# Performance work log

Hardware: AMD Instinct MI355X
Metric: run time of the kernel (lower is better)

## Reference

```python
import jax, jax.numpy as jnp
import numpy as np

N_NODES = 100000
N_EDGES = 1600000
D_IN = 64
D_OUT = 64


def setup_inputs() -> dict:
    key = jax.random.key(0)
    k1, k2, k3, k4, k5 = jax.random.split(key, 5)
    features = jax.random.normal(k1, (N_NODES, D_IN), dtype=jnp.float32)
    edge_rows = jax.random.randint(k2, (N_EDGES,), 0, N_NODES, dtype=jnp.int32)
    edge_cols = jax.random.randint(k3, (N_EDGES,), 0, N_NODES, dtype=jnp.int32)
    edge_vals = jax.random.uniform(k4, (N_EDGES,), dtype=jnp.float32)
    # glorot_uniform init for the dense projection weight
    limit = np.sqrt(6.0 / (D_IN + D_OUT)).astype(np.float32)
    weight = jax.random.uniform(k5, (D_IN, D_OUT), dtype=jnp.float32,
                                minval=-limit, maxval=limit)
    return {"features": features, "edge_rows": edge_rows,
            "edge_cols": edge_cols, "edge_vals": edge_vals, "weight": weight}


def reference(features, edge_rows, edge_cols, edge_vals, weight):
    # SpMM: (adj @ features) via edge-list gather + segment_sum
    gathered = features[edge_cols] * edge_vals[:, None]        # [E, D_IN]
    agg = jax.ops.segment_sum(gathered, edge_rows,
                              num_segments=N_NODES)            # [N, D_IN]
    # Dense projection + ReLU
    return jax.nn.relu(agg @ weight)                           # [N, D_OUT]
```

## Files before the change

### kernel.cpp

```cpp
#include <hip/hip_runtime.h>

#define D 64
#define OVF_CAP 65536


__device__ inline unsigned short f32_to_bf16_rne(float x) {
    unsigned u = __float_as_uint(x);
    unsigned r = (u + 0x7FFFu + ((u >> 16) & 1u)) >> 16;
    return (unsigned short)r;
}

__global__ void f2bf_kernel(const float4* __restrict__ in,
                            ushort4* __restrict__ out, int n4) {
    int i = blockIdx.x * blockDim.x + threadIdx.x;
    int stride = gridDim.x * blockDim.x;
    for (; i < n4; i += stride) {
        float4 f = in[i];
        ushort4 u;
        u.x = f32_to_bf16_rne(f.x);
        u.y = f32_to_bf16_rne(f.y);
        u.z = f32_to_bf16_rne(f.z);
        u.w = f32_to_bf16_rne(f.w);
        out[i] = u;
    }
}

template <int SLOTS, int NSLICE>
__global__ void scatter_slot_kernel(const int* __restrict__ erows,
                                    const int* __restrict__ ecols,
                                    const float* __restrict__ evals,
                                    int* __restrict__ cnt,
                                    int2* __restrict__ pairs,
                                    int4* __restrict__ ovf,
                                    int* __restrict__ ovfCnt,
                                    int n_edges, int rows_per_slice) {
    const int slice = blockIdx.x & (NSLICE - 1);
    const int rlo   = slice * rows_per_slice;
    const int rhi   = rlo + rows_per_slice;
    const int sub   = blockIdx.x / NSLICE;
    const int t     = sub * blockDim.x + threadIdx.x;
    const int strid = (gridDim.x / NSLICE) * blockDim.x;

    auto handle = [&](int r, int c, float v) {
        if (r >= rlo && r < rhi) {
            int pos = atomicAdd(&cnt[r], 1);
            if (pos < SLOTS) {
                pairs[(size_t)r * SLOTS + pos] = make_int2(c, __float_as_int(v));
            } else {
                int oi = atomicAdd(ovfCnt, 1);
                if (oi < OVF_CAP) ovf[oi] = make_int4(r, c, __float_as_int(v), 0);
            }
        }
    };

    int e = t;
    for (; e + 3 * strid < n_edges; e += 4 * strid) {
        int e0 = e, e1 = e + strid, e2 = e + 2 * strid, e3 = e + 3 * strid;
        int   r0 = erows[e0], r1 = erows[e1], r2 = erows[e2], r3 = erows[e3];
        int   c0 = ecols[e0], c1 = ecols[e1], c2 = ecols[e2], c3 = ecols[e3];
        float v0 = evals[e0], v1 = evals[e1], v2 = evals[e2], v3 = evals[e3];
        handle(r0, c0, v0);
        handle(r1, c1, v1);
        handle(r2, c2, v2);
        handle(r3, c3, v3);
    }
    for (; e < n_edges; e += strid)
        handle(erows[e], ecols[e], evals[e]);
}

template <int SLOTS>
__global__ void __launch_bounds__(256)
fused_slot_bf16(const unsigned short* __restrict__ fb,
                const int* __restrict__ cnt, const int2* __restrict__ pairs,
                const float* __restrict__ W, const int* __restrict__ ovfCnt,
                float* __restrict__ out, int n_rows) {
    __shared__ float sW[D * D];
    __shared__ float srow[4][D];

    for (int i = threadIdx.x; i < D * D; i += 256)
        sW[i] = W[i];

    const int  w      = threadIdx.x >> 6;
    const int  lane   = threadIdx.x & 63;
    const int  row    = blockIdx.x * 4 + w;
    const bool doRelu = (*ovfCnt == 0);

    float acc = 0.0f;
    if (row < n_rows) {
        int m = min(cnt[row], SLOTS);
        int px = 0, py = 0;
        if (lane < m) {
            int2 p = pairs[(size_t)row * SLOTS + lane];
            px = p.x; py = p.y;
        }
        int k = 0;
        for (; k + 4 <= m; k += 4) {
            int c0 = __shfl(px, k + 0), b0 = __shfl(py, k + 0);
            int c1 = __shfl(px, k + 1), b1 = __shfl(py, k + 1);
            int c2 = __shfl(px, k + 2), b2 = __shfl(py, k + 2);
            int c3 = __shfl(px, k + 3), b3 = __shfl(py, k + 3);
            float f0 = __uint_as_float((unsigned)fb[(size_t)c0 * D + lane] << 16);
            float f1 = __uint_as_float((unsigned)fb[(size_t)c1 * D + lane] << 16);
            float f2 = __uint_as_float((unsigned)fb[(size_t)c2 * D + lane] << 16);
            float f3 = __uint_as_float((unsigned)fb[(size_t)c3 * D + lane] << 16);
            acc = fmaf(f0, __int_as_float(b0), acc);
            acc = fmaf(f1, __int_as_float(b1), acc);
            acc = fmaf(f2, __int_as_float(b2), acc);
            acc = fmaf(f3, __int_as_float(b3), acc);
        }
        for (; k < m; ++k) {
            int c = __shfl(px, k), b = __shfl(py, k);
            acc = fmaf(__uint_as_float((unsigned)fb[(size_t)c * D + lane] << 16),
                       __int_as_float(b), acc);
        }
    }
    srow[w][lane] = acc;
    __syncthreads();

    float o = 0.0f;
#pragma unroll
    for (int kk = 0; kk < D; ++kk)
        o = fmaf(srow[w][kk], sW[kk * D + lane], o);

    if (row < n_rows)
        out[(size_t)row * D + lane] = doRelu ? fmaxf(o, 0.0f) : o;
}

template <int SLOTS>
__global__ void __launch_bounds__(256)
fused_slot_f32(const float* __restrict__ feat, const int* __restrict__ cnt,
               const int2* __restrict__ pairs, const float* __restrict__ W,
               const int* __restrict__ ovfCnt, float* __restrict__ out,
               int n_rows) {
    __shared__ float sW[D * D];
    __shared__ float srow[4][D];
    for (int i = threadIdx.x; i < D * D; i += 256) sW[i] = W[i];
    const int  w      = threadIdx.x >> 6;
    const int  lane   = threadIdx.x & 63;
    const int  row    = blockIdx.x * 4 + w;
    const bool doRelu = (*ovfCnt == 0);
    float acc = 0.0f;
    if (row < n_rows) {
        int m = min(cnt[row], SLOTS);
        int px = 0, py = 0;
        if (lane < m) {
            int2 p = pairs[(size_t)row * SLOTS + lane];
            px = p.x; py = p.y;
        }
        int k = 0;
        for (; k + 4 <= m; k += 4) {
            int c0 = __shfl(px, k + 0), b0 = __shfl(py, k + 0);
            int c1 = __shfl(px, k + 1), b1 = __shfl(py, k + 1);
            int c2 = __shfl(px, k + 2), b2 = __shfl(py, k + 2);
            int c3 = __shfl(px, k + 3), b3 = __shfl(py, k + 3);
            float f0 = feat[(size_t)c0 * D + lane];
            float f1 = feat[(size_t)c1 * D + lane];
            float f2 = feat[(size_t)c2 * D + lane];
            float f3 = feat[(size_t)c3 * D + lane];
            acc = fmaf(f0, __int_as_float(b0), acc);
            acc = fmaf(f1, __int_as_float(b1), acc);
            acc = fmaf(f2, __int_as_float(b2), acc);
            acc = fmaf(f3, __int_as_float(b3), acc);
        }
        for (; k < m; ++k) {
            int c = __shfl(px, k), b = __shfl(py, k);
            acc = fmaf(feat[(size_t)c * D + lane], __int_as_float(b), acc);
        }
    }
    srow[w][lane] = acc;
    __syncthreads();
    float o = 0.0f;
#pragma unroll
    for (int kk = 0; kk < D; ++kk)
        o = fmaf(srow[w][kk], sW[kk * D + lane], o);
    if (row < n_rows)
        out[(size_t)row * D + lane] = doRelu ? fmaxf(o, 0.0f) : o;
}

__global__ void __launch_bounds__(256)
ovf_kernel(const float* __restrict__ feat, const float* __restrict__ W,
           const int4* __restrict__ ovf, const int* __restrict__ ovfCnt,
           float* __restrict__ out) {
    int n = *ovfCnt;
    if (n > OVF_CAP) n = OVF_CAP;
    if (n == 0) return;
    const int lane = threadIdx.x & 63;
    const int wave = (blockIdx.x * blockDim.x + threadIdx.x) >> 6;
    const int nw   = (gridDim.x * blockDim.x) >> 6;
    for (int i = wave; i < n; i += nw) {
        int4  e = ovf[i];
        float v = __int_as_float(e.z);
        float f = feat[(size_t)e.y * D + lane];
        float acc = 0.0f;
#pragma unroll
        for (int k = 0; k < D; ++k)
            acc = fmaf(__shfl(f, k), W[k * D + lane], acc);
        unsafeAtomicAdd(&out[(size_t)e.x * D + lane], v * acc);
    }
}

__global__ void relu_fix_kernel(float* __restrict__ out,
                                const int* __restrict__ ovfCnt, int n_elems) {
    if (*ovfCnt == 0) return;
    int i = blockIdx.x * blockDim.x + threadIdx.x;
    int stride = gridDim.x * blockDim.x;
    for (; i < n_elems; i += stride)
        out[i] = fmaxf(out[i], 0.0f);
}

__global__ void hist_kernel(const int* __restrict__ erows, int* __restrict__ cur,
                            int n_edges) {
    int i = blockIdx.x * blockDim.x + threadIdx.x;
    int stride = gridDim.x * blockDim.x;
    for (int e = i; e < n_edges; e += stride) atomicAdd(&cur[erows[e]], 1);
}

__global__ void __launch_bounds__(256)
scan_block_reduce(const int* __restrict__ cnt, int* __restrict__ bs, int n) {
    __shared__ int s[256];
    int i = blockIdx.x * 256 + threadIdx.x;
    s[threadIdx.x] = (i < n) ? cnt[i] : 0;
    __syncthreads();
    for (int off = 128; off > 0; off >>= 1) {
        if (threadIdx.x < (unsigned)off) s[threadIdx.x] += s[threadIdx.x + off];
        __syncthreads();
    }
    if (threadIdx.x == 0) bs[blockIdx.x] = s[0];
}

__global__ void __launch_bounds__(1024)
scan_top(int* __restrict__ bs, int nblk, int* __restrict__ rowStartN) {
    __shared__ int s[1024];
    int t = threadIdx.x;
    int x = (t < nblk) ? bs[t] : 0;
    s[t] = x;
    __syncthreads();
    for (int off = 1; off < 1024; off <<= 1) {
        int y = (t >= off) ? s[t - off] : 0;
        __syncthreads();
        s[t] += y;
        __syncthreads();
    }
    if (t < nblk) bs[t] = s[t] - x;
    if (t == 1023) *rowStartN = s[1023];
}

__global__ void __launch_bounds__(256)
scan_final(int* __restrict__ cur, const int* __restrict__ bs,
           int* __restrict__ rowStart, int n) {
    __shared__ int s[256];
    int t = threadIdx.x;
    int i = blockIdx.x * 256 + t;
    int x = (i < n) ? cur[i] : 0;
    s[t] = x;
    __syncthreads();
    for (int off = 1; off < 256; off <<= 1) {
        int y = (t >= off) ? s[t - off] : 0;
        __syncthreads();
        s[t] += y;
        __syncthreads();
    }
    int excl = s[t] - x + bs[blockIdx.x];
    if (i < n) { rowStart[i] = excl; cur[i] = excl; }
}

__global__ void scatter_kernel(const int* __restrict__ erows,
                               const int* __restrict__ ecols,
                               const float* __restrict__ evals,
                               int* __restrict__ cur, int2* __restrict__ pairs,
                               int n_edges) {
    int i = blockIdx.x * blockDim.x + threadIdx.x;
    int stride = gridDim.x * blockDim.x;
    for (int e = i; e < n_edges; e += stride) {
        int pos = atomicAdd(&cur[erows[e]], 1);
        pairs[pos] = make_int2(ecols[e], __float_as_int(evals[e]));
    }
}

__global__ void __launch_bounds__(256)
fused_kernel(const float* __restrict__ feat, const int* __restrict__ rowStart,
             const int2* __restrict__ pairs, const float* __restrict__ W,
             float* __restrict__ out, int n_rows) {
    __shared__ float sW[D * D];
    __shared__ float srow[4][D];
    for (int i = threadIdx.x; i < D * D; i += 256) sW[i] = W[i];
    const int w = threadIdx.x >> 6, lane = threadIdx.x & 63;
    const int row = blockIdx.x * 4 + w;
    float acc = 0.0f;
    if (row < n_rows) {
        int s = rowStart[row], e = rowStart[row + 1], i = s;
        for (; i + 4 <= e; i += 4) {
            int2 p0 = pairs[i + 0], p1 = pairs[i + 1];
            int2 p2 = pairs[i + 2], p3 = pairs[i + 3];
            float f0 = feat[(size_t)p0.x * D + lane];
            float f1 = feat[(size_t)p1.x * D + lane];
            float f2 = feat[(size_t)p2.x * D + lane];
            float f3 = feat[(size_t)p3.x * D + lane];
            acc = fmaf(f0, __int_as_float(p0.y), acc);
            acc = fmaf(f1, __int_as_float(p1.y), acc);
            acc = fmaf(f2, __int_as_float(p2.y), acc);
            acc = fmaf(f3, __int_as_float(p3.y), acc);
        }
        for (; i < e; ++i) {
            int2 p = pairs[i];
            acc = fmaf(feat[(size_t)p.x * D + lane], __int_as_float(p.y), acc);
        }
    }
    srow[w][lane] = acc;
    __syncthreads();
    float o = 0.0f;
#pragma unroll
    for (int k = 0; k < D; ++k) o = fmaf(srow[w][k], sW[k * D + lane], o);
    if (row < n_rows) out[(size_t)row * D + lane] = fmaxf(o, 0.0f);
}

__global__ void agg_kernel(const float* __restrict__ feat,
                           const int* __restrict__ erows,
                           const int* __restrict__ ecols,
                           const float* __restrict__ evals,
                           float* __restrict__ agg, int n_edges) {
    int gid = blockIdx.x * blockDim.x + threadIdx.x;
    int group = gid >> 4, lane4 = gid & 15;
    int stride = (gridDim.x * blockDim.x) >> 4;
    for (int e = group; e < n_edges; e += stride) {
        int r = erows[e], c = ecols[e];
        float v = evals[e];
        const float4 f = *reinterpret_cast<const float4*>(feat + (size_t)c * D + lane4 * 4);
        float* dst = agg + (size_t)r * D + lane4 * 4;
        unsafeAtomicAdd(dst + 0, f.x * v);
        unsafeAtomicAdd(dst + 1, f.y * v);
        unsafeAtomicAdd(dst + 2, f.z * v);
        unsafeAtomicAdd(dst + 3, f.w * v);
    }
}

__global__ void __launch_bounds__(256)
proj_kernel(const float* __restrict__ agg, const float* __restrict__ W,
            float* __restrict__ out, int n_rows) {
    __shared__ float sW[D * D];
    __shared__ float srow[4][D];
    for (int i = threadIdx.x; i < D * D; i += 256) sW[i] = W[i];
    __syncthreads();
    const int rg = threadIdx.x >> 6, j = threadIdx.x & 63;
    for (int row0 = blockIdx.x * 4; row0 < n_rows; row0 += gridDim.x * 4) {
        int r = row0 + rg;
        float v = (r < n_rows) ? agg[(size_t)r * D + j] : 0.0f;
        srow[rg][j] = v;
        __syncthreads();
        float acc = 0.0f;
#pragma unroll
        for (int k = 0; k < D; ++k) acc = fmaf(srow[rg][k], sW[k * D + j], acc);
        if (r < n_rows) out[(size_t)r * D + j] = fmaxf(acc, 0.0f);
        __syncthreads();
    }
}

extern "C" void kernel_launch(void* const* d_in, const int* in_sizes, int n_in,
                              void* d_out, int out_size, void* d_ws, size_t ws_size,
                              hipStream_t stream) {
    const float* feat  = (const float*)d_in[0];
    const int*   erows = (const int*)  d_in[1];
    const int*   ecols = (const int*)  d_in[2];
    const float* evals = (const float*)d_in[3];
    const float* W     = (const float*)d_in[4];
    float*       out   = (float*)d_out;

    const int n_edges = in_sizes[1];
    const int n_nodes = in_sizes[0] / D;

    auto align256 = [](size_t x) { return (x + 255) & ~(size_t)255; };

    size_t off_cnt    = 0;
    size_t off_ovfCnt = align256((size_t)n_nodes * 4);
    size_t off_ovf    = align256(off_ovfCnt + 4);
    size_t off_fb     = align256(off_ovf + (size_t)OVF_CAP * 16);
    size_t off_pairs  = align256(off_fb + (size_t)n_nodes * D * 2);
    size_t need_bf16  = off_pairs + (size_t)n_nodes * 32 * 8;
    size_t off_pairs2 = off_fb;
    size_t need_f32   = off_pairs2 + (size_t)n_nodes * 32 * 8;

    const int rows_per_slice8 = (n_nodes + 7) / 8;
    const int nblk_fused      = (n_nodes + 3) / 4;

    if (ws_size >= need_bf16 || ws_size >= need_f32) {
        char* ws     = (char*)d_ws;
        int*  cnt    = (int*) (ws + off_cnt);
        int*  ovfCnt = (int*) (ws + off_ovfCnt);
        int4* ovf    = (int4*)(ws + off_ovf);

        hipMemsetAsync(cnt, 0, (size_t)n_nodes * 4, stream);
        hipMemsetAsync(ovfCnt, 0, 4, stream);

        if (ws_size >= need_bf16) {
            unsigned short* fb = (unsigned short*)(ws + off_fb);
            int2* pairs = (int2*)(ws + off_pairs);
            f2bf_kernel<<<2048, 256, 0, stream>>>(
                (const float4*)feat, (ushort4*)fb, n_nodes * D / 4);
            scatter_slot_kernel<32, 8><<<2048, 256, 0, stream>>>(
                erows, ecols, evals, cnt, pairs, ovf, ovfCnt, n_edges, rows_per_slice8);
            fused_slot_bf16<32><<<nblk_fused, 256, 0, stream>>>(
                fb, cnt, pairs, W, ovfCnt, out, n_nodes);
        } else {
            int2* pairs = (int2*)(ws + off_pairs2);
            scatter_slot_kernel<32, 8><<<2048, 256, 0, stream>>>(
                erows, ecols, evals, cnt, pairs, ovf, ovfCnt, n_edges, rows_per_slice8);
            fused_slot_f32<32><<<nblk_fused, 256, 0, stream>>>(
                feat, cnt, pairs, W, ovfCnt, out, n_nodes);
        }
        ovf_kernel<<<256, 256, 0, stream>>>(feat, W, ovf, ovfCnt, out);
        relu_fix_kernel<<<512, 256, 0, stream>>>(out, ovfCnt, n_nodes * D);
        return;
    }

    const int nblk = (n_nodes + 255) / 256;
    size_t off_rowStart = 0;
    size_t off_cur      = align256(off_rowStart + (size_t)(n_nodes + 1) * 4);
    size_t off_bs       = align256(off_cur + (size_t)n_nodes * 4);
    size_t off_p        = align256(off_bs + (size_t)nblk * 4);
    size_t ws_needed    = off_p + (size_t)n_edges * 8;

    if (ws_size >= ws_needed && nblk <= 1024) {
        char* ws = (char*)d_ws;
        int*  rowStart = (int*) (ws + off_rowStart);
        int*  cur      = (int*) (ws + off_cur);
        int*  bs       = (int*) (ws + off_bs);
        int2* pairs    = (int2*)(ws + off_p);

        hipMemsetAsync(cur, 0, (size_t)n_nodes * 4, stream);
        hist_kernel<<<2048, 256, 0, stream>>>(erows, cur, n_edges);
        scan_block_reduce<<<nblk, 256, 0, stream>>>(cur, bs, n_nodes);
        scan_top<<<1, 1024, 0, stream>>>(bs, nblk, rowStart + n_nodes);
        scan_final<<<nblk, 256, 0, stream>>>(cur, bs, rowStart, n_nodes);
        scatter_kernel<<<2048, 256, 0, stream>>>(erows, ecols, evals, cur, pairs, n_edges);
        fused_kernel<<<(n_nodes + 3) / 4, 256, 0, stream>>>(feat, rowStart, pairs, W, out, n_nodes);
    } else {
        hipMemsetAsync(out, 0, (size_t)n_nodes * D * 4, stream);
        agg_kernel<<<2048, 256, 0, stream>>>(feat, erows, ecols, evals, out, n_edges);
        proj_kernel<<<2048, 256, 0, stream>>>(out, W, out, n_nodes);
    }
}
```

Measured before the change: 295.2 us.

## Project features by W before aggregation and gather projected bf16 rows

Uses associativity, (A·X)·W = A·(X·W), to compute the dense projection once per node into a bf16 buffer G. The aggregation kernel then gathers G directly, with no per-row shared-memory matmul, and each wave handles two rows at once with interleaved accumulators. The scatter kernel now loads columns and values only for edges whose row falls in its slice, and it launches twice as many blocks. Rounding the projected values to bf16, instead of the raw features, can change the numerical error profile.

Result: faster. 273.1 us (-7.5%).

```diff
diff --git a/kernel.cpp b/kernel.cpp
--- a/kernel.cpp
+++ b/kernel.cpp
@@ -9,19 +9,28 @@
     unsigned r = (u + 0x7FFFu + ((u >> 16) & 1u)) >> 16;
     return (unsigned short)r;
 }
-
-__global__ void f2bf_kernel(const float4* __restrict__ in,
-                            ushort4* __restrict__ out, int n4) {
-    int i = blockIdx.x * blockDim.x + threadIdx.x;
-    int stride = gridDim.x * blockDim.x;
-    for (; i < n4; i += stride) {
-        float4 f = in[i];
-        ushort4 u;
-        u.x = f32_to_bf16_rne(f.x);
-        u.y = f32_to_bf16_rne(f.y);
-        u.z = f32_to_bf16_rne(f.z);
-        u.w = f32_to_bf16_rne(f.w);
-        out[i] = u;
+__device__ inline float bf16_to_f32(unsigned short h) {
+    return __uint_as_float((unsigned)h << 16);
+}
+
+__global__ void __launch_bounds__(256)
+gw_kernel(const float* __restrict__ feat, const float* __restrict__ W,
+          unsigned short* __restrict__ G, int n_rows) {
+    __shared__ float sW[D * D];
+    __shared__ float srow[4][D];
+    for (int i = threadIdx.x; i < D * D; i += 256) sW[i] = W[i];
+    __syncthreads();
+    const int rg = threadIdx.x >> 6, j = threadIdx.x & 63;
+    for (int row0 = blockIdx.x * 4; row0 < n_rows; row0 += gridDim.x * 4) {
+        int r = row0 + rg;
+        float v = (r < n_rows) ? feat[(size_t)r * D + j] : 0.0f;
+        srow[rg][j] = v;
+        __syncthreads();
+        float acc = 0.0f;
+#pragma unroll
+        for (int k = 0; k < D; ++k) acc = fmaf(srow[rg][k], sW[k * D + j], acc);
+        if (r < n_rows) G[(size_t)r * D + j] = f32_to_bf16_rne(acc);
+        __syncthreads();
     }
 }
 
@@ -41,89 +50,139 @@
     const int t     = sub * blockDim.x + threadIdx.x;
     const int strid = (gridDim.x / NSLICE) * blockDim.x;
 
-    auto handle = [&](int r, int c, float v) {
-        if (r >= rlo && r < rhi) {
-            int pos = atomicAdd(&cnt[r], 1);
-            if (pos < SLOTS) {
-                pairs[(size_t)r * SLOTS + pos] = make_int2(c, __float_as_int(v));
-            } else {
-                int oi = atomicAdd(ovfCnt, 1);
-                if (oi < OVF_CAP) ovf[oi] = make_int4(r, c, __float_as_int(v), 0);
-            }
+    auto handle = [&](int e, int r) {
+        int   c = ecols[e];
+        float v = evals[e];
+        int pos = atomicAdd(&cnt[r], 1);
+        if (pos < SLOTS) {
+            pairs[(size_t)r * SLOTS + pos] = make_int2(c, __float_as_int(v));
+        } else {
+            int oi = atomicAdd(ovfCnt, 1);
+            if (oi < OVF_CAP) ovf[oi] = make_int4(r, c, __float_as_int(v), 0);
         }
     };
 
     int e = t;
     for (; e + 3 * strid < n_edges; e += 4 * strid) {
-        int e0 = e, e1 = e + strid, e2 = e + 2 * strid, e3 = e + 3 * strid;
-        int   r0 = erows[e0], r1 = erows[e1], r2 = erows[e2], r3 = erows[e3];
-        int   c0 = ecols[e0], c1 = ecols[e1], c2 = ecols[e2], c3 = ecols[e3];
-        float v0 = evals[e0], v1 = evals[e1], v2 = evals[e2], v3 = evals[e3];
-        handle(r0, c0, v0);
-        handle(r1, c1, v1);
-        handle(r2, c2, v2);
-        handle(r3, c3, v3);
-    }
-    for (; e < n_edges; e += strid)
-        handle(erows[e], ecols[e], evals[e]);
+        int r0 = erows[e];
+        int r1 = erows[e + strid];
+        int r2 = erows[e + 2 * strid];
+        int r3 = erows[e + 3 * strid];
+        if (r0 >= rlo && r0 < rhi) handle(e, r0);
+        if (r1 >= rlo && r1 < rhi) handle(e + strid, r1);
+        if (r2 >= rlo && r2 < rhi) handle(e + 2 * strid, r2);
+        if (r3 >= rlo && r3 < rhi) handle(e + 3 * strid, r3);
+    }
+    for (; e < n_edges; e += strid) {
+        int r = erows[e];
+        if (r >= rlo && r < rhi) handle(e, r);
+    }
 }
 
 template <int SLOTS>
 __global__ void __launch_bounds__(256)
-fused_slot_bf16(const unsigned short* __restrict__ fb,
-                const int* __restrict__ cnt, const int2* __restrict__ pairs,
-                const float* __restrict__ W, const int* __restrict__ ovfCnt,
-                float* __restrict__ out, int n_rows) {
-    __shared__ float sW[D * D];
-    __shared__ float srow[4][D];
-
-    for (int i = threadIdx.x; i < D * D; i += 256)
-        sW[i] = W[i];
-
-    const int  w      = threadIdx.x >> 6;
+fused_gather2(const unsigned short* __restrict__ G, const int* __restrict__ cnt,
+              const int2* __restrict__ pairs, const int* __restrict__ ovfCnt,
+              float* __restrict__ out, int n_rows) {
     const int  lane   = threadIdx.x & 63;
-    const int  row    = blockIdx.x * 4 + w;
+    const int  slot   = lane & (SLOTS - 1);
+    const int  half   = lane >> 5;
+    const int  wid    = (blockIdx.x * blockDim.x + threadIdx.x) >> 6;
+    const int  nw     = (gridDim.x * blockDim.x) >> 6;
     const bool doRelu = (*ovfCnt == 0);
 
-    float acc = 0.0f;
-    if (row < n_rows) {
-        int m = min(cnt[row], SLOTS);
-        int px = 0, py = 0;
-        if (lane < m) {
-            int2 p = pairs[(size_t)row * SLOTS + lane];
-            px = p.x; py = p.y;
-        }
+    for (int base = wid * 2; base < n_rows; base += nw * 2) {
+        const int r0 = base, r1 = base + 1;
+        int m0 = min(cnt[r0], SLOTS);
+        int m1 = (r1 < n_rows) ? min(cnt[r1], SLOTS) : 0;
+
+        int2 p = make_int2(0, 0);
+        if (r0 + half < n_rows)
+            p = pairs[(size_t)r0 * SLOTS + lane];
+        const int mh = half ? m1 : m0;
+        int px = (slot < mh) ? p.x : 0;
+        int py = (slot < mh) ? p.y : 0;
+
+        float acc0 = 0.0f, acc1 = 0.0f;
+        const int mm = max(m0, m1);
         int k = 0;
-        for (; k + 4 <= m; k += 4) {
-            int c0 = __shfl(px, k + 0), b0 = __shfl(py, k + 0);
-            int c1 = __shfl(px, k + 1), b1 = __shfl(py, k + 1);
-            int c2 = __shfl(px, k + 2), b2 = __shfl(py, k + 2);
-            int c3 = __shfl(px, k + 3), b3 = __shfl(py, k + 3);
-            float f0 = __uint_as_float((unsigned)fb[(size_t)c0 * D + lane] << 16);
-            float f1 = __uint_as_float((unsigned)fb[(size_t)c1 * D + lane] << 16);
-            float f2 = __uint_as_float((unsigned)fb[(size_t)c2 * D + lane] << 16);
-            float f3 = __uint_as_float((unsigned)fb[(size_t)c3 * D + lane] << 16);
-            acc = fmaf(f0, __int_as_float(b0), acc);
-            acc = fmaf(f1, __int_as_float(b1), acc);
-            acc = fmaf(f2, __int_as_float(b2), acc);
-            acc = fmaf(f3, __int_as_float(b3), acc);
-        }
-        for (; k < m; ++k) {
-            int c = __shfl(px, k), b = __shfl(py, k);
-            acc = fmaf(__uint_as_float((unsigned)fb[(size_t)c * D + lane] << 16),
-                       __int_as_float(b), acc);
-        }
-    }
-    srow[w][lane] = acc;
-    __syncthreads();
-
-    float o = 0.0f;
-#pragma unroll
-    for (int kk = 0; kk < D; ++kk)
-        o = fmaf(srow[w][kk], sW[kk * D + lane], o);
-
-    if (row < n_rows)
-        out[(size_t)row * D + lane] = doRelu ? fmaxf(o, 0.0f) : o;
+        for (; k + 4 <= mm; k += 4) {
+#pragma unroll
+            for (int u = 0; u < 4; u += 2) {
+                int cA0 = __shfl(px, k + u),          bA0 = __shfl(py, k + u);
+                int cB0 = __shfl(px, 32 + k + u),     bB0 = __shfl(py, 32 + k + u);
+                int cA1 = __shfl(px, k + u + 1),      bA1 = __shfl(py, k + u + 1);
+                int cB1 = __shfl(px, 32 + k + u + 1), bB1 = __shfl(py, 32 + k + u + 1);
+                float fA0 = bf16_to_f32(G[(size_t)cA0 * D + lane]);
+                float fB0 = bf16_to_f32(G[(size_t)cB0 * D + lane]);
+                float fA1 = bf16_to_f32(G[(size_t)cA1 * D + lane]);
+                float fB1 = bf16_to_f32(G[(size_t)cB1 * D + lane]);
+                acc0 = fmaf(fA0, __int_as_float(bA0), acc0);
+                acc1 = fmaf(fB0, __int_as_float(bB0), acc1);
+                acc0 = fmaf(fA1, __int_as_float(bA1), acc0);
+                acc1 = fmaf(fB1, __int_as_float(bB1), acc1);
+            }
+        }
+        for (; k < mm; ++k) {
+            int cA = __shfl(px, k),      bA = __shfl(py, k);
+            int cB = __shfl(px, 32 + k), bB = __shfl(py, 32 + k);
+            float fA = bf16_to_f32(G[(size_t)cA * D + lane]);
+            float fB = bf16_to_f32(G[(size_t)cB * D + lane]);
+            acc0 = fmaf(fA, __int_as_float(bA), acc0);
+            acc1 = fmaf(fB, __int_as_float(bB), acc1);
+        }
+
+        out[(size_t)r0 * D + lane] = doRelu ? fmaxf(acc0, 0.0f) : acc0;
+        if (r1 < n_rows)
+            out[(size_t)r1 * D + lane] = doRelu ? fmaxf(acc1, 0.0f) : acc1;
+    }
+}
+
+__global__ void __launch_bounds__(256)
+ovf_kernel_g(const unsigned short* __restrict__ G, const int4* __restrict__ ovf,
+             const int* __restrict__ ovfCnt, float* __restrict__ out) {
+    int n = *ovfCnt;
+    if (n > OVF_CAP) n = OVF_CAP;
+    if (n == 0) return;
+    const int lane = threadIdx.x & 63;
+    const int wave = (blockIdx.x * blockDim.x + threadIdx.x) >> 6;
+    const int nw   = (gridDim.x * blockDim.x) >> 6;
+    for (int i = wave; i < n; i += nw) {
+        int4  e = ovf[i];
+        float g = bf16_to_f32(G[(size_t)e.y * D + lane]);
+        unsafeAtomicAdd(&out[(size_t)e.x * D + lane], __int_as_float(e.z) * g);
+    }
+}
+
+__global__ void __launch_bounds__(256)
+ovf_kernel_fw(const float* __restrict__ feat, const float* __restrict__ W,
+              const int4* __restrict__ ovf, const int* __restrict__ ovfCnt,
+              float* __restrict__ out) {
+    int n = *ovfCnt;
+    if (n > OVF_CAP) n = OVF_CAP;
+    if (n == 0) return;
+    const int lane = threadIdx.x & 63;
+    const int wave = (blockIdx.x * blockDim.x + threadIdx.x) >> 6;
+    const int nw   = (gridDim.x * blockDim.x) >> 6;
+    for (int i = wave; i < n; i += nw) {
+        int4  e = ovf[i];
+        float v = __int_as_float(e.z);
+        float f = feat[(size_t)e.y * D + lane];
+        float acc = 0.0f;
+#pragma unroll
+        for (int k = 0; k < D; ++k)
+            acc = fmaf(__shfl(f, k), W[k * D + lane], acc);
+        unsafeAtomicAdd(&out[(size_t)e.x * D + lane], v * acc);
+    }
+}
+
+__global__ void relu_fix_kernel(float* __restrict__ out,
+                                const int* __restrict__ ovfCnt, int n_elems) {
+    if (*ovfCnt == 0) return;
+    int i = blockIdx.x * blockDim.x + threadIdx.x;
+    int stride = gridDim.x * blockDim.x;
+    for (; i < n_elems; i += stride)
+        out[i] = fmaxf(out[i], 0.0f);
 }
 
 template <int SLOTS>
@@ -175,37 +234,6 @@
         o = fmaf(srow[w][kk], sW[kk * D + lane], o);
     if (row < n_rows)
         out[(size_t)row * D + lane] = doRelu ? fmaxf(o, 0.0f) : o;
-}
-
-__global__ void __launch_bounds__(256)
-ovf_kernel(const float* __restrict__ feat, const float* __restrict__ W,
-           const int4* __restrict__ ovf, const int* __restrict__ ovfCnt,
-           float* __restrict__ out) {
-    int n = *ovfCnt;
-    if (n > OVF_CAP) n = OVF_CAP;
-    if (n == 0) return;
-    const int lane = threadIdx.x & 63;
-    const int wave = (blockIdx.x * blockDim.x + threadIdx.x) >> 6;
-    const int nw   = (gridDim.x * blockDim.x) >> 6;
-    for (int i = wave; i < n; i += nw) {
-        int4  e = ovf[i];
-        float v = __int_as_float(e.z);
-        float f = feat[(size_t)e.y * D + lane];
-        float acc = 0.0f;
-#pragma unroll
-        for (int k = 0; k < D; ++k)
-            acc = fmaf(__shfl(f, k), W[k * D + lane], acc);
-        unsafeAtomicAdd(&out[(size_t)e.x * D + lane], v * acc);
-    }
-}
-
-__global__ void relu_fix_kernel(float* __restrict__ out,
-                                const int* __restrict__ ovfCnt, int n_elems) {
-    if (*ovfCnt == 0) return;
-    int i = blockIdx.x * blockDim.x + threadIdx.x;
-    int stride = gridDim.x * blockDim.x;
-    for (; i < n_elems; i += stride)
-        out[i] = fmaxf(out[i], 0.0f);
 }
 
 __global__ void hist_kernel(const int* __restrict__ erows, int* __restrict__ cur,
@@ -373,14 +401,13 @@
     size_t off_cnt    = 0;
     size_t off_ovfCnt = align256((size_t)n_nodes * 4);
     size_t off_ovf    = align256(off_ovfCnt + 4);
-    size_t off_fb     = align256(off_ovf + (size_t)OVF_CAP * 16);
-    size_t off_pairs  = align256(off_fb + (size_t)n_nodes * D * 2);
+    size_t off_G      = align256(off_ovf + (size_t)OVF_CAP * 16);
+    size_t off_pairs  = align256(off_G + (size_t)n_nodes * D * 2);
     size_t need_bf16  = off_pairs + (size_t)n_nodes * 32 * 8;
-    size_t off_pairs2 = off_fb;
+    size_t off_pairs2 = off_G;
     size_t need_f32   = off_pairs2 + (size_t)n_nodes * 32 * 8;
 
     const int rows_per_slice8 = (n_nodes + 7) / 8;
-    const int nblk_fused      = (n_nodes + 3) / 4;
 
     if (ws_size >= need_bf16 || ws_size >= need_f32) {
         char* ws     = (char*)d_ws;
@@ -392,22 +419,22 @@
         hipMemsetAsync(ovfCnt, 0, 4, stream);
 
         if (ws_size >= need_bf16) {
-            unsigned short* fb = (unsigned short*)(ws + off_fb);
+            unsigned short* G = (unsigned short*)(ws + off_G);
             int2* pairs = (int2*)(ws + off_pairs);
-            f2bf_kernel<<<2048, 256, 0, stream>>>(
-                (const float4*)feat, (ushort4*)fb, n_nodes * D / 4);
-            scatter_slot_kernel<32, 8><<<2048, 256, 0, stream>>>(
+            gw_kernel<<<2048, 256, 0, stream>>>(feat, W, G, n_nodes);
+            scatter_slot_kernel<32, 8><<<4096, 256, 0, stream>>>(
                 erows, ecols, evals, cnt, pairs, ovf, ovfCnt, n_edges, rows_per_slice8);
-            fused_slot_bf16<32><<<nblk_fused, 256, 0, stream>>>(
-                fb, cnt, pairs, W, ovfCnt, out, n_nodes);
+            fused_gather2<32><<<2048, 256, 0, stream>>>(
+                G, cnt, pairs, ovfCnt, out, n_nodes);
+            ovf_kernel_g<<<256, 256, 0, stream>>>(G, ovf, ovfCnt, out);
         } else {
             int2* pairs = (int2*)(ws + off_pairs2);
-            scatter_slot_kernel<32, 8><<<2048, 256, 0, stream>>>(
+            scatter_slot_kernel<32, 8><<<4096, 256, 0, stream>>>(
                 erows, ecols, evals, cnt, pairs, ovf, ovfCnt, n_edges, rows_per_slice8);
-            fused_slot_f32<32><<<nblk_fused, 256, 0, stream>>>(
+            fused_slot_f32<32><<<(n_nodes + 3) / 4, 256, 0, stream>>>(
                 feat, cnt, pairs, W, ovfCnt, out, n_nodes);
-        }
-        ovf_kernel<<<256, 256, 0, stream>>>(feat, W, ovf, ovfCnt, out);
+            ovf_kernel_fw<<<256, 256, 0, stream>>>(feat, W, ovf, ovfCnt, out);
+        }
         relu_fix_kernel<<<512, 256, 0, stream>>>(out, ovfCnt, n_nodes * D);
         return;
     }
```
